# Optimization experiments

Hardware: AMD Instinct MI355X
Metric: run time of the kernel (lower is better)

The kernel has to match this reference:

```python
import jax, jax.numpy as jnp
import numpy as np
from jax import lax

EPS = 1e-5
NUM_HEADS = 8
HEAD_DIM = 64
NUM_DEVICES = 8
MAX_DEV = 3       # max_devices_per_token
TOP_K = 6         # num_experts_per_tok
EBF, DBF, CBF = 0.003, 0.05, 0.02  # aux loss factors


def rms_norm(x, eps=EPS):
    xf = x.astype(jnp.float32)
    var = jnp.mean(jnp.square(xf), axis=-1, keepdims=True)
    return (xf * lax.rsqrt(var + eps)).astype(x.dtype)


def rotate_half(x):
    x1, x2 = jnp.split(x, 2, axis=-1)
    return jnp.concatenate([-x2, x1], axis=-1)


def swiglu(x, wgu, wd):
    gate, up = jnp.split(x @ wgu, 2, axis=-1)
    return (jax.nn.silu(gate) * up) @ wd


def attention(x, w_qkv, w_o, cos, sin):
    B, S, H = x.shape
    qkv = (x @ w_qkv).reshape(B, S, 3 * NUM_HEADS, HEAD_DIM)
    q, k, v = (qkv[:, :, :NUM_HEADS], qkv[:, :, NUM_HEADS:2 * NUM_HEADS],
               qkv[:, :, 2 * NUM_HEADS:])
    c = cos[None, :, None, :]
    s = sin[None, :, None, :]
    q = q * c + rotate_half(q) * s
    k = k * c + rotate_half(k) * s
    scores = jnp.einsum('bqhd,bkhd->bhqk', q, k) / np.float32(np.sqrt(HEAD_DIM))
    p = jax.nn.softmax(scores, axis=-1)  # non-causal
    o = jnp.einsum('bhqk,bkhd->bqhd', p, v).reshape(B, S, H)
    return o @ w_o


def deepseek_moe(x, router_w, r_wgu, r_wd, s_wgu, s_wd):
    B, S, H = x.shape
    E = router_w.shape[1]
    epd = E // NUM_DEVICES
    e2d = jnp.arange(E) // epd  # expert -> device (contiguous blocks)

    logits = x @ router_w                         # [B,S,E]
    probs = jax.nn.softmax(logits, axis=-1)
    # device-limited routing (max_devices_per_token < num_devices)
    dev_scores = probs.reshape(B, S, NUM_DEVICES, epd).sum(-1)  # [B,S,D]
    _, sel_dev = lax.top_k(dev_scores, MAX_DEV)                 # [B,S,3]
    allowed = (sel_dev[..., :, None] == e2d[None, None, None, :]).any(-2)  # [B,S,E]
    masked = jnp.where(allowed, probs, -jnp.inf)
    w, idx = lax.top_k(masked, TOP_K)             # [B,S,K]
    w = jax.nn.softmax(w, axis=-1)

    T = B * S
    xf = x.reshape(T, H)
    idx_f = idx.reshape(T, TOP_K)
    # combine weights [T,E]: scatter-add top-k weights per token
    cw = jnp.zeros((T, E), x.dtype).at[jnp.arange(T)[:, None], idx_f].add(
        w.reshape(T, TOP_K))
    # accumulate weighted expert outputs, streaming one expert at a time
    def body(acc, we):
        wgu, wd, c = we
        return acc + c[:, None] * swiglu(xf, wgu, wd), None
    routed, _ = lax.scan(body, jnp.zeros_like(xf), (r_wgu, r_wd, cw.T))
    routed = routed.reshape(B, S, H)

    shared = swiglu(x, s_wgu[0], s_wd[0]) + swiglu(x, s_wgu[1], s_wd[1])
    out = x + shared + routed

    # auxiliary losses
    f_i = jnp.zeros(E, jnp.float32).at[idx.reshape(-1)].add(1.0) / (T * TOP_K)
    P_i = probs.astype(jnp.float32).mean((0, 1))
    expert_bal = (f_i * P_i).sum() * EBF
    dev_f = f_i.reshape(NUM_DEVICES, epd).mean(-1)
    dev_P = P_i.reshape(NUM_DEVICES, epd).sum(-1)
    device_bal = (dev_f * dev_P).sum() * DBF
    dev_sel = e2d[idx]  # [B,S,K]
    counts = jnp.zeros(NUM_DEVICES, jnp.float32).at[dev_sel.reshape(-1)].add(1.0)
    f_comm = counts / (T * MAX_DEV)
    comm_bal = (f_comm * dev_P).sum() * CBF
    return out, expert_bal, device_bal, comm_bal


def setup_inputs() -> dict:
    key = jax.random.key(0)
    ks = jax.random.split(key, 8)
    B, S, H, E = 4, 1024, 512, 64
    INTER = 1536  # _find_multiple(round(512*4*2/3), 256)
    sc = 1.0 / np.sqrt(H)
    sci = 1.0 / np.sqrt(INTER)
    # RoPE tables
    inv_freq = 1.0 / (10000.0 ** (np.arange(0, HEAD_DIM, 2) / HEAD_DIM))
    freqs = np.outer(np.arange(S), inv_freq)
    emb = np.concatenate([freqs, freqs], axis=-1)
    return {
        'hidden_states': jax.random.normal(ks[0], (B, S, H), jnp.float32),
        'cos': jnp.asarray(np.cos(emb), jnp.float32),
        'sin': jnp.asarray(np.sin(emb), jnp.float32),
        'w_qkv': jax.random.normal(ks[1], (H, 3 * H), jnp.float32) * sc,
        'w_o': jax.random.normal(ks[2], (H, H), jnp.float32) * sc,
        'router_w': jax.random.normal(ks[3], (H, E), jnp.float32) * sc,
        'r_wgu': jax.random.normal(ks[4], (E, H, 2 * INTER), jnp.float32) * sc,
        'r_wd': jax.random.normal(ks[5], (E, INTER, H), jnp.float32) * sci,
        's_wgu': jax.random.normal(ks[6], (2, H, 2 * INTER), jnp.float32) * sc,
        's_wd': jax.random.normal(ks[7], (2, INTER, H), jnp.float32) * sci,
    }


def reference(hidden_states, cos, sin, w_qkv, w_o, router_w, r_wgu, r_wd,
              s_wgu, s_wd):
    h = rms_norm(hidden_states + attention(hidden_states, w_qkv, w_o, cos, sin))
    moe_out, ebl, dbl, cbl = deepseek_moe(h, router_w, r_wgu, r_wd, s_wgu, s_wd)
    h = rms_norm(moe_out)
    return h, ebl, dbl, cbl, ebl + dbl + cbl
```

## Files before the change

kernel.cpp:

```cpp
#include <hip/hip_runtime.h>
#include <math.h>

#define TOK   4096
#define SEQL  1024
#define HID   512
#define NEXP  64
#define FFI   1536

typedef short bf16x8v __attribute__((ext_vector_type(8)));
typedef float f32x4   __attribute__((ext_vector_type(4)));

__device__ __forceinline__ unsigned short f2bf(float f){
  unsigned int u = __float_as_uint(f);
  u += 0x7fffu + ((u >> 16) & 1u);
  return (unsigned short)(u >> 16);
}
__device__ __forceinline__ float bf2f(unsigned short s){
  return __uint_as_float(((unsigned int)s) << 16);
}
__device__ __forceinline__ void split2(float v, unsigned short& h, unsigned short& l){
  h = f2bf(v);
  l = f2bf(v - bf2f(h));
}
__device__ __forceinline__ void gload16(const void* g, void* l){
// ... 42 lines not shown
    for (int j=0;j<8;j++) split2(tile[rq+j][c], th[j], tl[j]);
    long long o = (long long)(c0+c)*R + r0 + rq;
    *(uint4*)&ohi[o] = *(uint4*)th;
    *(uint4*)&olo[o] = *(uint4*)tl;
  }
}

template<bool PAIRED>
__global__ __launch_bounds__(256) void kconvT(const float* __restrict__ in,
    unsigned short* __restrict__ out, int R, int C){
  __shared__ float tile[64][65];
  long long zb = (long long)blockIdx.z * R * C;
  int c0 = blockIdx.x*64, r0 = blockIdx.y*64;
  int tid = threadIdx.x;
  #pragma unroll
  for (int it=0; it<4; it++){
    int idx = it*256+tid; int r = idx>>4; int cq = (idx&15)*4;
    float4 v = *(const float4*)&in[zb + (long long)(r0+r)*C + c0 + cq];
    tile[r][cq]=v.x; tile[r][cq+1]=v.y; tile[r][cq+2]=v.z; tile[r][cq+3]=v.w;
  }
  __syncthreads();
  #pragma unroll
  for (int it=0; it<2; it++){
    int idx = it*256+tid; int c = idx>>3; int rq=(idx&7)*8;
    unsigned short tb[8] __attribute__((aligned(16)));
    #pragma unroll
    for (int j=0;j<8;j++) tb[j] = f2bf(tile[rq+j][c]);
    int cc = c0 + c;
    int orow = PAIRED ? ((cc < (C>>1)) ? 2*cc : 2*(cc-(C>>1))+1) : cc;
    *(uint4*)&out[zb + (long long)orow*R + r0 + rq] = *(uint4*)tb;
  }
}

template<int WM,int WN,int FM,int FN,int SPLIT>
__global__ __launch_bounds__(256) void gemm_x3(
    const unsigned short* __restrict__ Ahi, const unsigned short* __restrict__ Alo,
    const unsigned short* __restrict__ Bhi, const unsigned short* __restrict__ Blo,
    float* __restrict__ C, unsigned short* __restrict__ OH, unsigned short* __restrict__ OL,
    int K, int lda, int ldb, int ldc, float alpha,
    long long a1, long long a2, int adiv,
    long long b1, long long b2, int bdiv,
    long long c1, long long c2, int cdiv)
{
  constexpr int BM = WM*FM*16, BN = WN*FN*16;
  constexpr int AIT = (2*BM*4)/256, BIT = (2*BN*4)/256;
  int z = blockIdx.z;
  long long aoff = (long long)(z/adiv)*a1 + (long long)(z%adiv)*a2;
  long long boff = (long long)(z/bdiv)*b1 + (long long)(z%bdiv)*b2;
  long long coff = (long long)(z/cdiv)*c1 + (long long)(z%cdiv)*c2;
  int m0 = blockIdx.x*BM, n0 = blockIdx.y*BN;
  __shared__ __align__(16) unsigned short As[2][BM*40];
  __shared__ __align__(16) unsigned short Bs[2][BN*40];
  int tid = threadIdx.x, lane = tid&63, wid = tid>>6;
  int wr = wid / WN, wc = wid % WN;
  int lrow = lane&15, kgo = (lane>>4)*8;
  f32x4 acc[FM][FN];
  #pragma unroll
  for (int mi=0;mi<FM;mi++)
    #pragma unroll
    for (int nj=0;nj<FN;nj++) acc[mi][nj] = (f32x4){0.f,0.f,0.f,0.f};

  for (int k0=0; k0<K; k0+=32){
    uint4 ta[AIT], tb[BIT];
    #pragma unroll
    for (int it=0; it<AIT; it++){
      int c = it*256+tid; int pl = c/(BM*4); int rem = c%(BM*4);
      int row = rem>>2, q = (rem&3)*8;
      const unsigned short* src = pl ? Alo : Ahi;
      ta[it] = *(const uint4*)&src[aoff + (long long)(m0+row)*lda + k0 + q];
    }
    #pragma unroll
// ... 17 lines not shown
      *(uint4*)&Bs[pl][row*40+q] = tb[it];
    }
    __syncthreads();
    bf16x8v ah[FM], al[FM], bh[FN], bl[FN];
    int ab = (wr*FM*16 + lrow)*40 + kgo;
    int bb = (wc*FN*16 + lrow)*40 + kgo;
    #pragma unroll
    for (int mi=0;mi<FM;mi++){
      ah[mi] = *(const bf16x8v*)&As[0][ab + mi*640];
      al[mi] = *(const bf16x8v*)&As[1][ab + mi*640];
    }
    #pragma unroll
    for (int nj=0;nj<FN;nj++){
      bh[nj] = *(const bf16x8v*)&Bs[0][bb + nj*640];
      bl[nj] = *(const bf16x8v*)&Bs[1][bb + nj*640];
    }
    #pragma unroll
    for (int mi=0;mi<FM;mi++)
      #pragma unroll
      for (int nj=0;nj<FN;nj++){
        acc[mi][nj] = __builtin_amdgcn_mfma_f32_16x16x32_bf16(ah[mi], bh[nj], acc[mi][nj], 0,0,0);
        acc[mi][nj] = __builtin_amdgcn_mfma_f32_16x16x32_bf16(ah[mi], bl[nj], acc[mi][nj], 0,0,0);
        acc[mi][nj] = __builtin_amdgcn_mfma_f32_16x16x32_bf16(al[mi], bh[nj], acc[mi][nj], 0,0,0);
      }
  }
  int crow = m0 + wr*FM*16 + ((lane>>4)<<2);
  int ccol = n0 + wc*FN*16 + (lane&15);
  #pragma unroll
  for (int mi=0;mi<FM;mi++)
    #pragma unroll
    for (int r=0;r<4;r++){
      long long row = crow + mi*16 + r;
      #pragma unroll
      for (int nj=0;nj<FN;nj++){
        float v = alpha*acc[mi][nj][r];
        if constexpr (SPLIT){
          unsigned short hh, ll;
          split2(v, hh, ll);
          OH[coff + row*ldc + ccol + nj*16] = hh;
          OL[coff + row*ldc + ccol + nj*16] = ll;
        } else {
          C[coff + row*ldc + ccol + nj*16] = v;
        }
      }
    }
}

__global__ __launch_bounds__(256) void krope(float* __restrict__ qkv,
    unsigned short* __restrict__ qhi, unsigned short* __restrict__ qlo,
    const float* __restrict__ cosb, const float* __restrict__ sinb){
  int gid = blockIdx.x*256 + threadIdx.x;
  int t = gid >> 8; int rem = gid & 255; int h = rem >> 5; int d = rem & 31;
  int s = t & (SEQL-1);
  long long base = (long long)t*1536 + h*64;
  float c1 = cosb[s*64+d], c2 = cosb[s*64+d+32];
  float s1 = sinb[s*64+d], s2 = sinb[s*64+d+32];
  float q1 = qkv[base+d], q2 = qkv[base+d+32];
  float rq1 = q1*c1 - q2*s1, rq2 = q2*c2 + q1*s2;
  qkv[base+d] = rq1; qkv[base+d+32] = rq2;
  split2(rq1, qhi[base+d],    qlo[base+d]);
  split2(rq2, qhi[base+d+32], qlo[base+d+32]);
  float k1 = qkv[base+512+d], k2 = qkv[base+512+d+32];
  float rk1 = k1*c1 - k2*s1, rk2 = k2*c2 + k1*s2;
  qkv[base+512+d] = rk1; qkv[base+512+d+32] = rk2;
  split2(rk1, qhi[base+512+d],    qlo[base+512+d]);
  split2(rk2, qhi[base+512+d+32], qlo[base+512+d+32]);
}

__global__ __launch_bounds__(256) void kvtrans(const float* __restrict__ qkv,
    unsigned short* __restrict__ vhi, unsigned short* __restrict__ vlo){
  __shared__ float tile[64][65];
  int s0 = blockIdx.x*64;
  int z = blockIdx.y;
  int b = z >> 3, h = z & 7;
  int tid = threadIdx.x;
  #pragma unroll
  for (int it=0; it<4; it++){
    int idx = it*256+tid; int r = idx>>4; int cq = (idx&15)*4;
    float4 v = *(const float4*)&qkv[((long long)(b*1024 + s0 + r))*1536 + 1024 + h*64 + cq];
    tile[r][cq]=v.x; tile[r][cq+1]=v.y; tile[r][cq+2]=v.z; tile[r][cq+3]=v.w;
  }
  __syncthreads();
  #pragma unroll
  for (int it=0; it<2; it++){
    int idx = it*256+tid; int d = idx>>3; int sq = (idx&7)*8;
    unsigned short th[8] __attribute__((aligned(16)));
    unsigned short tl[8] __attribute__((aligned(16)));
    #pragma unroll
    for (int j=0;j<8;j++) split2(tile[sq+j][d], th[j], tl[j]);
    long long o = ((long long)(z*64 + d))*1024 + s0 + sq;
    *(uint4*)&vhi[o] = *(uint4*)th;
    *(uint4*)&vlo[o] = *(uint4*)tl;
  }
}

__global__ __launch_bounds__(256) void ksoftmax(const float* __restrict__ sc,
    unsigned short* __restrict__ phi, unsigned short* __restrict__ plo){
  long long row = blockIdx.x;
  const float* p = sc + row*1024;
  int tid = threadIdx.x;
  float4 v = *(const float4*)&p[tid*4];
  float m = fmaxf(fmaxf(v.x,v.y), fmaxf(v.z,v.w));
  for (int o=32;o>0;o>>=1) m = fmaxf(m, __shfl_xor(m,o));
  __shared__ float redm[4], reds[4];
  int wid = tid>>6, lane = tid&63;
  if (lane==0) redm[wid]=m;
  __syncthreads();
  m = fmaxf(fmaxf(redm[0],redm[1]), fmaxf(redm[2],redm[3]));
  float e0=expf(v.x-m), e1=expf(v.y-m), e2=expf(v.z-m), e3=expf(v.w-m);
  float sum = e0+e1+e2+e3;
  for (int o=32;o>0;o>>=1) sum += __shfl_xor(sum,o);
  if (lane==0) reds[wid]=sum;
  __syncthreads();
  sum = reds[0]+reds[1]+reds[2]+reds[3];
  float inv = 1.0f/sum;
  unsigned short h0,h1,h2,h3,l0,l1,l2,l3;
  split2(e0*inv,h0,l0); split2(e1*inv,h1,l1); split2(e2*inv,h2,l2); split2(e3*inv,h3,l3);
  *(ushort4*)&phi[row*1024 + tid*4] = make_ushort4(h0,h1,h2,h3);
  *(ushort4*)&plo[row*1024 + tid*4] = make_ushort4(l0,l1,l2,l3);
}

__global__ __launch_bounds__(128) void krms1(const float* __restrict__ x, const float* __restrict__ attn,
    unsigned short* __restrict__ h1hi, unsigned short* __restrict__ h1lo,
    unsigned short* __restrict__ h1b, float* __restrict__ hbuf){
  long long row = blockIdx.x;
  int tid = threadIdx.x;
  float4 xv = *(const float4*)&x[row*512 + tid*4];
  float4 av = *(const float4*)&attn[row*512 + tid*4];
  float4 v; v.x=xv.x+av.x; v.y=xv.y+av.y; v.z=xv.z+av.z; v.w=xv.w+av.w;
  float ss = v.x*v.x + v.y*v.y + v.z*v.z + v.w*v.w;
  for (int o=32;o>0;o>>=1) ss += __shfl_xor(ss,o);
  __shared__ float red[2];
  int wid = tid>>6, lane = tid&63;
  if (lane==0) red[wid]=ss;
  __syncthreads();
  ss = red[0]+red[1];
  float r = 1.0f/sqrtf(ss*(1.0f/512.0f) + 1e-5f);
  float4 o; o.x=v.x*r; o.y=v.y*r; o.z=v.z*r; o.w=v.w*r;
  *(float4*)&hbuf[row*512 + tid*4] = o;
  unsigned short h0,h1,h2,h3,l0,l1,l2,l3;
  split2(o.x,h0,l0); split2(o.y,h1,l1); split2(o.z,h2,l2); split2(o.w,h3,l3);
  *(ushort4*)&h1hi[row*512 + tid*4] = make_ushort4(h0,h1,h2,h3);
  *(ushort4*)&h1lo[row*512 + tid*4] = make_ushort4(l0,l1,l2,l3);
  *(ushort4*)&h1b[row*512 + tid*4] = make_ushort4(f2bf(o.x),f2bf(o.y),f2bf(o.z),f2bf(o.w));
}

__device__ void route_decide(float p, int e, int t,
    int* __restrict__ idx, float* __restrict__ wts,
    int* __restrict__ flagcnt, int* __restrict__ flaglist){
  float d = p;
  d += __shfl_xor(d,1); d += __shfl_xor(d,2); d += __shfl_xor(d,4);
  int g = e >> 3;
  float gs[8];
  #pragma unroll
  for (int j=0;j<8;j++) gs[j] = __shfl(d, j*8);
  int rank = 0;
  #pragma unroll
  for (int j=0;j<8;j++) rank += (gs[j] > d) || (gs[j] == d && j < g);
  float q = (rank < 3) ? p : -INFINITY;
  float svals[7]; int sidx[7];
  #pragma unroll
  for (int kk=0; kk<7; kk++){
    float v = q; int vi = e;
    for (int o=32;o>0;o>>=1){
      float ov = __shfl_xor(v,o); int oi = __shfl_xor(vi,o);
      if (ov > v || (ov == v && oi < vi)){ v = ov; vi = oi; }
    }
    svals[kk] = v; sidx[kk] = vi;
    if (e == vi) q = -INFINITY;
  }
  float mx = svals[0], tot = 0.f, wv[6];
  #pragma unroll
  for (int kk=0;kk<6;kk++){ wv[kk] = expf(svals[kk]-mx); tot += wv[kk]; }
  if (e < 6){
    idx[t*6+e] = sidx[e];
    wts[t*6+e] = wv[e]/tot;
  }
  if (flagcnt != nullptr && e == 0){
    float a[8];
    #pragma unroll
    for (int j=0;j<8;j++) a[j] = gs[j];
    float t3=-1e30f, t4=-1e30f;
    for (int it2=0; it2<4; it2++){
      int bi=0; float bv=a[0];
      #pragma unroll
      for (int j=1;j<8;j++) if (a[j] > bv){ bv=a[j]; bi=j; }
      if (it2==2) t3=bv;
      if (it2==3) t4=bv;
      a[bi] = -1e30f;
    }
    float pgap = svals[5] - svals[6];
    float dgap = t3 - t4;
    if (pgap < 1e-4f || dgap < 5e-4f){
      int pos = atomicAdd(flagcnt, 1);
      if (pos < 1024) flaglist[pos] = t;
    }
  }
}

__global__ __launch_bounds__(256) void krouter(const float* __restrict__ logits,
    float* __restrict__ probs, int* __restrict__ idx, float* __restrict__ wts,
    int* __restrict__ flagcnt, int* __restrict__ flaglist){
  int t = blockIdx.x*4 + (threadIdx.x >> 6);
  int e = threadIdx.x & 63;
  float l = logits[t*64 + e];
  float m = l;
  for (int o=32;o>0;o>>=1) m = fmaxf(m, __shfl_xor(m,o));
  float p = expf(l-m);
  float s = p;
  for (int o=32;o>0;o>>=1) s += __shfl_xor(s,o);
  p /= s;
  probs[t*64+e] = p;
  route_decide(p, e, t, idx, wts, flagcnt, flaglist);
}

__global__ __launch_bounds__(256) void kfix_attn(const int* __restrict__ flagcnt,
    const int* __restrict__ flaglist, const float* __restrict__ qkv, float* __restrict__ fixo){
  int fc = *flagcnt; if (fc > 1024) fc = 1024;
  if ((int)blockIdx.x >= fc) return;
  int t = flaglist[blockIdx.x];
  int h = blockIdx.y;
  int b = t >> 10;
  int tid = threadIdx.x, lane = tid & 63, w = tid >> 6;
  __shared__ float sc[1024];
  __shared__ float qh[64];
  __shared__ float red[4];
  __shared__ float op[4][64];
  __shared__ float sinv;
  if (tid < 64) qh[tid] = qkv[(long long)t*1536 + h*64 + tid];
  __syncthreads();
  float q = qh[lane];
  const float* kb = qkv + (long long)b*1024*1536 + 512 + h*64 + lane;
  for (int s0 = w*256; s0 < w*256 + 256; s0 += 8){
    float p[8];
    #pragma unroll
    for (int j=0;j<8;j++) p[j] = q * kb[(long long)(s0+j)*1536];
    #pragma unroll
    for (int o=32;o>0;o>>=1){
      #pragma unroll
      for (int j=0;j<8;j++) p[j] += __shfl_xor(p[j],o);
    }
    if (lane == 0){
      #pragma unroll
      for (int j=0;j<8;j++) sc[s0+j] = p[j] * 0.125f;
    }
  }
// ... 1 lines not shown
  float m = -1e30f;
  for (int s = tid; s < 1024; s += 256) m = fmaxf(m, sc[s]);
  #pragma unroll
  for (int o=32;o>0;o>>=1) m = fmaxf(m, __shfl_xor(m,o));
  if (lane == 0) red[w] = m;
  __syncthreads();
  m = fmaxf(fmaxf(red[0],red[1]), fmaxf(red[2],red[3]));
  __syncthreads();
  float sum = 0.f;
  for (int s = tid; s < 1024; s += 256){ float e = expf(sc[s]-m); sc[s] = e; sum += e; }
  #pragma unroll
  for (int o=32;o>0;o>>=1) sum += __shfl_xor(sum,o);
  if (lane == 0) red[w] = sum;
  __syncthreads();
  if (tid == 0) sinv = 1.0f/(red[0]+red[1]+red[2]+red[3]);
  const float* vb = qkv + (long long)b*1024*1536 + 1024 + h*64 + lane;
  float a0 = 0.f, a1 = 0.f, a2 = 0.f, a3 = 0.f;
  for (int s = w*256; s < w*256 + 256; s += 4){
    a0 += sc[s]   * vb[(long long)(s)*1536];
    a1 += sc[s+1] * vb[(long long)(s+1)*1536];
    a2 += sc[s+2] * vb[(long long)(s+2)*1536];
    a3 += sc[s+3] * vb[(long long)(s+3)*1536];
  }
  op[w][lane] = (a0+a1)+(a2+a3);
  __syncthreads();
  if (tid < 64)
    fixo[(long long)blockIdx.x*512 + h*64 + tid] =
      (op[0][tid]+op[1][tid]+op[2][tid]+op[3][tid]) * sinv;
}

__global__ __launch_bounds__(256) void kfix_route(const int* __restrict__ flagcnt,
    const int* __restrict__ flaglist, const float* __restrict__ fixo,
    const float* __restrict__ x, const float* __restrict__ w_o, const float* __restrict__ router_w,
    int* __restrict__ idx, float* __restrict__ wts, float* __restrict__ probs){
  int fc = *flagcnt; if (fc > 1024) fc = 1024;
  if ((int)blockIdx.x >= fc) return;
  int t = flaglist[blockIdx.x];
  int tid = threadIdx.x;
  __shared__ float o512[512];
  __shared__ float h1s[512];
  __shared__ float red[4];
  o512[tid]     = fixo[(long long)blockIdx.x*512 + tid];
  o512[tid+256] = fixo[(long long)blockIdx.x*512 + tid + 256];
  __syncthreads();
  int j0 = tid, j1 = tid + 256;
  float a0 = 0.f, a1 = 0.f;
  #pragma unroll 4
  for (int i = 0; i < 512; i++){
    float oi = o512[i];
    a0 += oi * w_o[(long long)i*512 + j0];
    a1 += oi * w_o[(long long)i*512 + j1];
  }
  float hj0 = x[(long long)t*512 + j0] + a0;
  float hj1 = x[(long long)t*512 + j1] + a1;
  float ss = hj0*hj0 + hj1*hj1;
  #pragma unroll
  for (int o=32;o>0;o>>=1) ss += __shfl_xor(ss,o);
  if ((tid&63)==0) red[tid>>6]=ss;
  __syncthreads();
  ss = red[0]+red[1]+red[2]+red[3];
  float r = 1.0f/sqrtf(ss*(1.0f/512.0f) + 1e-5f);
  h1s[j0] = hj0*r; h1s[j1] = hj1*r;
  __syncthreads();
  if (tid < 64){
    int e = tid;
    float le = 0.f;
    #pragma unroll 4
    for (int i=0;i<512;i++) le += h1s[i]*router_w[(long long)i*64 + e];
    float m2 = le;
    #pragma unroll
    for (int o=32;o>0;o>>=1) m2 = fmaxf(m2, __shfl_xor(m2,o));
    float p = expf(le - m2), s2 = p;
    #pragma unroll
    for (int o=32;o>0;o>>=1) s2 += __shfl_xor(s2,o);
    p /= s2;
    probs[(long long)t*64 + e] = p;
    route_decide(p, e, t, idx, wts, nullptr, nullptr);
  }
}

__global__ void kcount(const int* __restrict__ idx, int* __restrict__ cnt){
  int g = blockIdx.x*256 + threadIdx.x;
  if (g < TOK*6) atomicAdd(&cnt[idx[g]], 1);
}

__global__ __launch_bounds__(256) void ksump(const float* __restrict__ probs, float* __restrict__ sumP){
  int e = blockIdx.x; int tid = threadIdx.x;
  float acc = 0.f;
  for (int t = tid; t < TOK; t += 256) acc += probs[t*64 + e];
  for (int o=32;o>0;o>>=1) acc += __shfl_xor(acc,o);
  __shared__ float red[4];
  int wid = tid>>6, lane = tid&63;
  if (lane==0) red[wid]=acc;
  __syncthreads();
  if (tid==0) sumP[e] = red[0]+red[1]+red[2]+red[3];
}

__global__ void kfinalize(const int* __restrict__ cnt, int* __restrict__ offs,
                          int2* __restrict__ tiles, int* __restrict__ ntl){
  int e = threadIdx.x;
  int c = cnt[e];
  int inc = c;
  #pragma unroll
  for (int o=1;o<64;o<<=1){ int v = __shfl_up(inc,o); if (e>=o) inc += v; }
  offs[e] = inc - c;
  if (e == 63) offs[64] = inc;
  int nte = (c + 127) >> 7;
  int tinc = nte;
  #pragma unroll
  for (int o=1;o<64;o<<=1){ int v = __shfl_up(tinc,o); if (e>=o) tinc += v; }
  int tbase = tinc - nte;
  for (int i=0;i<nte;i++) tiles[tbase+i] = make_int2(e, i*128);
  if (e == 63) *ntl = tinc;
}

__global__ __launch_bounds__(256) void kscatter(const int* __restrict__ idx, const float* __restrict__ wts,
    const int* __restrict__ offs, int* __restrict__ cursor,
    int* __restrict__ rowsl, float* __restrict__ wrowl, int* __restrict__ slot_of){
  int g = blockIdx.x*256 + threadIdx.x;
  if (g >= TOK*6) return;
  int t = g/6, kk = g%6;
  int e = idx[t*6+kk];
  int pos = atomicAdd(&cursor[e], 1);
  int slot = offs[e]+pos;
  rowsl[slot] = t;
  wrowl[slot] = wts[t*6+kk];
  slot_of[t*6+kk] = slot;
}

__global__ __launch_bounds__(256) void kgather(const unsigned short* __restrict__ h1b,
    const int* __restrict__ rowsl, unsigned short* __restrict__ xg){
  int r = blockIdx.x*4 + (threadIdx.x>>6);
  int lane = threadIdx.x&63;
  int tok = rowsl[r];
  *(uint4*)&xg[(long long)r*512 + lane*8] = *(const uint4*)&h1b[(long long)tok*512 + lane*8];
}

template<int MODE>
__global__ __launch_bounds__(256) void gemm_ffn(
    const unsigned short* __restrict__ Ab, const unsigned short* __restrict__ Bw,
    unsigned short* __restrict__ Cact, float* __restrict__ Cd,
    const int* __restrict__ offs, const int2* __restrict__ tiles, const int* __restrict__ ntl,
    int N, int K)
{
  int e=0, m0=0, roff=0, Me=1<<30, n0=0, zi=0;
  long long Aoff=0, Boff=0;
  int lda;
  if constexpr (MODE==0 || MODE==1){
    constexpr int NF = (MODE==0) ? 24 : 4;
    int nt = *ntl;
    int total = nt*NF;
    int l = xcd_swizzle(blockIdx.x, total);
    if (l < 0 || l >= total) return;
    int tile = l / NF; int y = l % NF;
    int2 tl = tiles[tile];
    e = tl.x; m0 = tl.y;
    roff = offs[e]; Me = offs[e+1]-roff;
    n0 = y*128;
    Boff = (long long)e*N*K;
    lda = K;
  } else {
    m0 = blockIdx.x*128;
    n0 = blockIdx.y*128;
    zi = blockIdx.z;
    Boff = (long long)zi*N*K;
    if constexpr (MODE==2) lda = 512;
    else { lda = K; Aoff = (long long)zi*4096LL*K; }
  }
  __shared__ __align__(16) unsigned short As[128*32];
  __shared__ __align__(16) unsigned short Bs[128*32];
  int tid = threadIdx.x, lane = tid&63, wid = tid>>6;
  int wr = wid>>1, wc = wid&1;
  int lrow = lane&15, kgo = (lane>>4)*8;
  f32x4 acc[4][4];
  #pragma unroll
  for (int mi=0;mi<4;mi++)
    #pragma unroll
    for (int nj=0;nj<4;nj++) acc[mi][nj] = (f32x4){0.f,0.f,0.f,0.f};

  int g0 = wid*2, g1 = wid*2 + 1;
  int colq = (lane&3)*8;
  int ar0 = g0*16 + (lane>>2), ar1 = g1*16 + (lane>>2);
  long long abase0, abase1;
  if constexpr (MODE==0 || MODE==1){
    int r0 = roff + m0 + ar0; if (r0 > 24575) r0 = 24575;
    int r1 = roff + m0 + ar1; if (r1 > 24575) r1 = 24575;
    abase0 = (long long)r0*lda; abase1 = (long long)r1*lda;
  } else if constexpr (MODE==2){
    abase0 = (long long)(m0+ar0)*lda; abase1 = (long long)(m0+ar1)*lda;
// ... 14 lines not shown
    int ab = (wr*64 + lrow)*32 + kgo;
    int bb = (wc*64 + lrow)*32 + kgo;
    #pragma unroll
    for (int mi=0;mi<4;mi++) af[mi]  = *(const bf16x8v*)&As[ab + mi*512];
    #pragma unroll
    for (int nj=0;nj<4;nj++) bfv[nj] = *(const bf16x8v*)&Bs[bb + nj*512];
    #pragma unroll
    for (int mi=0;mi<4;mi++)
      #pragma unroll
      for (int nj=0;nj<4;nj++)
        acc[mi][nj] = __builtin_amdgcn_mfma_f32_16x16x32_bf16(af[mi], bfv[nj], acc[mi][nj], 0,0,0);
  }

  int lq = lane>>4;
  int l15 = lane&15;
  if constexpr (MODE==0 || MODE==2){
    bool evenlane = (l15&1)==0;
    int pb = (n0>>1) + wc*32 + (l15>>1);
    #pragma unroll
    for (int mi=0;mi<4;mi++){
      #pragma unroll
      for (int r2=0;r2<4;r2++){
        int lr = wr*64 + mi*16 + lq*4 + r2;
        bool valid; long long grow;
        if constexpr (MODE==0){ valid = (m0+lr)<Me; grow = roff+m0+lr; }
        else { valid = true; grow = (long long)zi*4096 + m0 + lr; }
        #pragma unroll
        for (int nj=0;nj<4;nj++){
          float v = acc[mi][nj][r2];
          float o2 = __shfl_xor(v,1);
          if (evenlane && valid){
            float g = v, u = o2;
            float sg = g/(1.0f+expf(-g))*u;
            Cact[grow*1536 + pb + nj*8] = f2bf(sg);
          }
        }
      }
    }
  } else {
    #pragma unroll
    for (int mi=0;mi<4;mi++)
      #pragma unroll
      for (int r2=0;r2<4;r2++){
        int lr = wr*64 + mi*16 + lq*4 + r2;
        bool valid; long long grow;
        if constexpr (MODE==1){ valid = (m0+lr)<Me; grow = roff+m0+lr; }
        else { valid = true; grow = (long long)zi*4096 + m0 + lr; }
        if (valid){
          #pragma unroll
          for (int nj=0;nj<4;nj++)
            Cd[grow*512 + n0 + wc*64 + nj*16 + l15] = acc[mi][nj][r2];
        }
      }
  }
}

__global__ __launch_bounds__(128) void kreduce(const float* __restrict__ hbuf,
    const float* __restrict__ sdout, const float* __restrict__ dout,
    const int* __restrict__ slot_of, const float* __restrict__ wts,
    float* __restrict__ out){
  int t = blockIdx.x;
  int tid = threadIdx.x;
  int c4 = tid*4;
  float4 s = *(const float4*)&hbuf[(long long)t*512 + c4];
  float4 a = *(const float4*)&sdout[(long long)t*512 + c4];
  float4 b = *(const float4*)&sdout[(long long)(4096+t)*512 + c4];
  s.x += a.x + b.x; s.y += a.y + b.y; s.z += a.z + b.z; s.w += a.w + b.w;
  #pragma unroll
  for (int kk=0; kk<6; kk++){
    float w = wts[t*6+kk];
    int slot = slot_of[t*6+kk];
    float4 d = *(const float4*)&dout[(long long)slot*512 + c4];
    s.x += w*d.x; s.y += w*d.y; s.z += w*d.z; s.w += w*d.w;
  }
  float ss = s.x*s.x + s.y*s.y + s.z*s.z + s.w*s.w;
  for (int o=32;o>0;o>>=1) ss += __shfl_xor(ss,o);
  __shared__ float red[2];
  int wid = tid>>6, lane = tid&63;
  if (lane==0) red[wid]=ss;
  __syncthreads();
  ss = red[0]+red[1];
  float r = 1.0f/sqrtf(ss*(1.0f/512.0f) + 1e-5f);
  float4 o; o.x=s.x*r; o.y=s.y*r; o.z=s.z*r; o.w=s.w*r;
  *(float4*)&out[(long long)t*512 + c4] = o;
}

__global__ void kscalars(const int* __restrict__ cnt, const float* __restrict__ sumP, float* __restrict__ o){
  int e = threadIdx.x;
  float cf = (float)cnt[e];
  float f = cf / 24576.0f;
  float P = sumP[e] / 4096.0f;
  float fg = f, Pg = P, cg = cf;
  fg += __shfl_xor(fg,1); fg += __shfl_xor(fg,2); fg += __shfl_xor(fg,4);
  Pg += __shfl_xor(Pg,1); Pg += __shfl_xor(Pg,2); Pg += __shfl_xor(Pg,4);
  cg += __shfl_xor(cg,1); cg += __shfl_xor(cg,2); cg += __shfl_xor(cg,4);
  float t1 = f*P;
  float t2 = ((e&7)==0) ? (fg/8.0f)*Pg : 0.0f;
  float t3 = ((e&7)==0) ? (cg/12288.0f)*Pg : 0.0f;
  for (int s=32;s>0;s>>=1){
    t1 += __shfl_xor(t1,s); t2 += __shfl_xor(t2,s); t3 += __shfl_xor(t3,s);
  }
  if (e==0){
    float ebl = t1*0.003f, dbl = t2*0.05f, cbl = t3*0.02f;
    o[0]=ebl; o[1]=dbl; o[2]=cbl; o[3]=ebl+dbl+cbl;
  }
}
// ... 16 lines not shown
  char* base = (char*)d_ws;
  size_t off = 0;
  auto alloc = [&](size_t b)->char*{
    char* p = base + off; off = (off + b + 255) & ~(size_t)255; return p;
  };
  unsigned short* x_hi   = (unsigned short*)alloc(2097152ULL*2);
  unsigned short* x_lo   = (unsigned short*)alloc(2097152ULL*2);
  unsigned short* wqkvT_hi = (unsigned short*)alloc(786432ULL*2);
  unsigned short* wqkvT_lo = (unsigned short*)alloc(786432ULL*2);
  unsigned short* woT_hi = (unsigned short*)alloc(262144ULL*2);
  unsigned short* woT_lo = (unsigned short*)alloc(262144ULL*2);
  unsigned short* wrT_hi = (unsigned short*)alloc(32768ULL*2);
  unsigned short* wrT_lo = (unsigned short*)alloc(32768ULL*2);
  unsigned short* h1_hi  = (unsigned short*)alloc(2097152ULL*2);
  unsigned short* h1_lo  = (unsigned short*)alloc(2097152ULL*2);
  unsigned short* h1b    = (unsigned short*)alloc(2097152ULL*2);
  float* hbuf   = (float*)alloc(2097152ULL*4);
  float* fixo   = (float*)alloc(1024ULL*512*4);
  float* logits = (float*)alloc(262144ULL*4);
  float* probs  = (float*)alloc(262144ULL*4);
  int*   idx    = (int*)alloc(24576ULL*4);
  float* wts    = (float*)alloc(24576ULL*4);
  int*   slot_of= (int*)alloc(24576ULL*4);
  int*   cnt     = (int*)alloc(256);
  int*   cursor  = (int*)alloc(256);
  int*   flagcnt = (int*)alloc(256);
  int*   flaglist= (int*)alloc(1024*4);
  int*   offs   = (int*)alloc(65*4);
  int*   ntl    = (int*)alloc(256);
  float* sumP   = (float*)alloc(64*4);
  int2*  tiles  = (int2*)alloc(512*8);
  int*   rowsl  = (int*)alloc(24576ULL*4);
  float* wrowl  = (float*)alloc(24576ULL*4);

  size_t region = off;
  size_t oA = region, oF = region;
  auto allocV = [&](size_t b, size_t& o2)->char*{
    char* p = base + o2; o2 = (o2 + b + 255) & ~(size_t)255; return p;
  };
  float* qkv    = (float*)allocV(6291456ULL*4, oA);
  unsigned short* qkv_hi = (unsigned short*)allocV(6291456ULL*2, oA);
  unsigned short* qkv_lo = (unsigned short*)allocV(6291456ULL*2, oA);
  unsigned short* vT_hi  = (unsigned short*)allocV(2097152ULL*2, oA);
  unsigned short* vT_lo  = (unsigned short*)allocV(2097152ULL*2, oA);
  float* scores = (float*)allocV(33554432ULL*4, oA);
  unsigned short* p_hi = (unsigned short*)allocV(33554432ULL*2, oA);
  unsigned short* p_lo = (unsigned short*)allocV(33554432ULL*2, oA);
  unsigned short* attno_hi = (unsigned short*)allocV(2097152ULL*2, oA);
  unsigned short* attno_lo = (unsigned short*)allocV(2097152ULL*2, oA);
  float* attnw = (float*)allocV(2097152ULL*4, oA);
  unsigned short* wguT = (unsigned short*)allocV(100663296ULL*2, oF);
  unsigned short* sguT = (unsigned short*)allocV(3145728ULL*2, oF);
  unsigned short* xg   = (unsigned short*)allocV(12582912ULL*2, oF);
  unsigned short* hact = (unsigned short*)allocV(37748736ULL*2, oF);
  unsigned short* shact= (unsigned short*)allocV(12582912ULL*2, oF);
  float* dout  = (float*)allocV(12582912ULL*4, oF);
  float* sdout = (float*)allocV(4194304ULL*4, oF);
  unsigned short* wdT  = wguT;
  unsigned short* swdT = wguT + 50331648ULL;

  hipMemsetAsync(cnt, 0, 768, stream);

  ksplit<<<2048, 256, 0, stream>>>(x, x_hi, x_lo, 524288);
  kTsplit<<<dim3(24,8), 256, 0, stream>>>(w_qkv, wqkvT_hi, wqkvT_lo, 512, 1536);
  kTsplit<<<dim3(8,8),  256, 0, stream>>>(w_o, woT_hi, woT_lo, 512, 512);
  kTsplit<<<dim3(1,8),  256, 0, stream>>>(router_w, wrT_hi, wrT_lo, 512, 64);

  gemm_x3<2,2,4,4,0><<<dim3(32,12,1), 256, 0, stream>>>(x_hi, x_lo, wqkvT_hi, wqkvT_lo,
      qkv, nullptr, nullptr, 512, 512, 512, 1536, 1.0f, 0,0,1, 0,0,1, 0,0,1);
  krope<<<4096, 256, 0, stream>>>(qkv, qkv_hi, qkv_lo, cosb, sinb);
  kvtrans<<<dim3(16,32), 256, 0, stream>>>(qkv, vT_hi, vT_lo);

  gemm_x3<2,2,4,4,0><<<dim3(8,8,32), 256, 0, stream>>>(qkv_hi, qkv_lo, qkv_hi+512, qkv_lo+512,
      scores, nullptr, nullptr, 64, 1536, 1536, 1024, 0.125f,
      1572864LL,64,8, 1572864LL,64,8, 1048576LL,0,1);
  ksoftmax<<<32768, 256, 0, stream>>>(scores, p_hi, p_lo);
  gemm_x3<2,2,2,2,1><<<dim3(16,1,32), 256, 0, stream>>>(p_hi, p_lo, vT_hi, vT_lo,
      nullptr, attno_hi, attno_lo, 1024, 1024, 1024, 512, 1.0f,
      1048576LL,0,1, 65536LL,0,1, 524288LL,64,8);
  gemm_x3<2,2,4,4,0><<<dim3(32,4,1), 256, 0, stream>>>(attno_hi, attno_lo, woT_hi, woT_lo,
      attnw, nullptr, nullptr, 512, 512, 512, 512, 1.0f, 0,0,1, 0,0,1, 0,0,1);
  krms1<<<4096, 128, 0, stream>>>(x, attnw, h1_hi, h1_lo, h1b, hbuf);
  gemm_x3<2,2,2,2,0><<<dim3(64,1,1), 256, 0, stream>>>(h1_hi, h1_lo, wrT_hi, wrT_lo,
      logits, nullptr, nullptr, 512, 512, 512, 64, 1.0f, 0,0,1, 0,0,1, 0,0,1);
  krouter<<<1024, 256, 0, stream>>>(logits, probs, idx, wts, flagcnt, flaglist);
  kfix_attn<<<dim3(1024,8), 256, 0, stream>>>(flagcnt, flaglist, qkv, fixo);
  kfix_route<<<1024, 256, 0, stream>>>(flagcnt, flaglist, fixo, x, w_o, router_w, idx, wts, probs);
  kcount<<<96, 256, 0, stream>>>(idx, cnt);
  ksump<<<64, 256, 0, stream>>>(probs, sumP);
  kfinalize<<<1, 64, 0, stream>>>(cnt, offs, tiles, ntl);
  kscatter<<<96, 256, 0, stream>>>(idx, wts, offs, cursor, rowsl, wrowl, slot_of);

  kgather<<<6144, 256, 0, stream>>>(h1b, rowsl, xg);
  kconvT<true><<<dim3(48,8,64), 256, 0, stream>>>(r_wgu, wguT, 512, 3072);
  kconvT<true><<<dim3(48,8,2),  256, 0, stream>>>(s_wgu, sguT, 512, 3072);
  gemm_ffn<0><<<6144, 256, 0, stream>>>(xg, wguT, hact, nullptr, offs, tiles, ntl, 3072, 512);
  gemm_ffn<2><<<dim3(32,24,2), 256, 0, stream>>>(h1b, sguT, shact, nullptr, offs, tiles, ntl, 3072, 512);
  kconvT<false><<<dim3(8,24,64), 256, 0, stream>>>(r_wd, wdT, 1536, 512);
  kconvT<false><<<dim3(8,24,2),  256, 0, stream>>>(s_wd, swdT, 1536, 512);
  gemm_ffn<1><<<1024, 256, 0, stream>>>(hact, wdT, nullptr, dout, offs, tiles, ntl, 512, 1536);
  gemm_ffn<3><<<dim3(32,4,2), 256, 0, stream>>>(shact, swdT, nullptr, sdout, offs, tiles, ntl, 512, 1536);

  kreduce<<<4096, 128, 0, stream>>>(hbuf, sdout, dout, slot_of, wts, out);
  kscalars<<<1, 64, 0, stream>>>(cnt, sumP, out + 2097152);
}
```

Before: 1.379 ms.

## Fuse attention into flash kernel, fold expert counting into router, store FFN outputs bf16

Replaces the separate scores GEMM, softmax and PV GEMM with a single flash-attention kernel that keeps scores in registers and shared memory, using an online softmax with split-bf16 MFMAs. This removes the large fp32 score buffer and the two bf16 probability buffers. Expert counting moves into the router via atomics, with corrections in the fix-up kernel, so the separate count kernel is gone. The down-projection outputs are also stored as bf16 instead of fp32, which halves that traffic but lowers output precision. The buffer allocation changes from overlapped regions to separate allocations.

```diff
diff --git a/kernel.cpp b/kernel.cpp
--- a/kernel.cpp
+++ b/kernel.cpp
@@ -98,11 +98,11 @@
   }
 }
 
-template<int WM,int WN,int FM,int FN,int SPLIT>
+template<int WM,int WN,int FM,int FN>
 __global__ __launch_bounds__(256) void gemm_x3(
     const unsigned short* __restrict__ Ahi, const unsigned short* __restrict__ Alo,
     const unsigned short* __restrict__ Bhi, const unsigned short* __restrict__ Blo,
-    float* __restrict__ C, unsigned short* __restrict__ OH, unsigned short* __restrict__ OL,
+    float* __restrict__ C,
     int K, int lda, int ldb, int ldc, float alpha,
     long long a1, long long a2, int adiv,
     long long b1, long long b2, int bdiv,
@@ -186,17 +186,8 @@
     for (int r=0;r<4;r++){
       long long row = crow + mi*16 + r;
       #pragma unroll
-      for (int nj=0;nj<FN;nj++){
-        float v = alpha*acc[mi][nj][r];
-        if constexpr (SPLIT){
-          unsigned short hh, ll;
-          split2(v, hh, ll);
-          OH[coff + row*ldc + ccol + nj*16] = hh;
-          OL[coff + row*ldc + ccol + nj*16] = ll;
-        } else {
-          C[coff + row*ldc + ccol + nj*16] = v;
-        }
-      }
+      for (int nj=0;nj<FN;nj++)
+        C[coff + row*ldc + ccol + nj*16] = alpha*acc[mi][nj][r];
     }
 }
 
@@ -248,30 +239,116 @@
   }
 }
 
-__global__ __launch_bounds__(256) void ksoftmax(const float* __restrict__ sc,
-    unsigned short* __restrict__ phi, unsigned short* __restrict__ plo){
-  long long row = blockIdx.x;
-  const float* p = sc + row*1024;
-  int tid = threadIdx.x;
-  float4 v = *(const float4*)&p[tid*4];
-  float m = fmaxf(fmaxf(v.x,v.y), fmaxf(v.z,v.w));
-  for (int o=32;o>0;o>>=1) m = fmaxf(m, __shfl_xor(m,o));
-  __shared__ float redm[4], reds[4];
-  int wid = tid>>6, lane = tid&63;
-  if (lane==0) redm[wid]=m;
-  __syncthreads();
-  m = fmaxf(fmaxf(redm[0],redm[1]), fmaxf(redm[2],redm[3]));
-  float e0=expf(v.x-m), e1=expf(v.y-m), e2=expf(v.z-m), e3=expf(v.w-m);
-  float sum = e0+e1+e2+e3;
-  for (int o=32;o>0;o>>=1) sum += __shfl_xor(sum,o);
-  if (lane==0) reds[wid]=sum;
-  __syncthreads();
-  sum = reds[0]+reds[1]+reds[2]+reds[3];
-  float inv = 1.0f/sum;
-  unsigned short h0,h1,h2,h3,l0,l1,l2,l3;
-  split2(e0*inv,h0,l0); split2(e1*inv,h1,l1); split2(e2*inv,h2,l2); split2(e3*inv,h3,l3);
-  *(ushort4*)&phi[row*1024 + tid*4] = make_ushort4(h0,h1,h2,h3);
-  *(ushort4*)&plo[row*1024 + tid*4] = make_ushort4(l0,l1,l2,l3);
+__global__ __launch_bounds__(256) void kflash(
+    const unsigned short* __restrict__ qkv_hi, const unsigned short* __restrict__ qkv_lo,
+    const unsigned short* __restrict__ vT_hi,  const unsigned short* __restrict__ vT_lo,
+    unsigned short* __restrict__ attno_hi, unsigned short* __restrict__ attno_lo)
+{
+  int qt = blockIdx.x;
+  int z  = blockIdx.y;
+  int b = z >> 3, h = z & 7;
+  int tid = threadIdx.x, lane = tid & 63, w = tid >> 6;
+  int q0 = qt*64 + w*16;
+  int fr = lane & 15;
+  int fk = (lane >> 4) * 8;
+
+  long long qbase  = ((long long)(b*1024 + q0 + fr))*1536 + h*64;
+  long long kbhb   = ((long long)b*1024)*1536 + 512 + h*64;
+  long long vbase  = ((long long)z*64)*1024;
+
+  bf16x8v qa_h[2], qa_l[2];
+  qa_h[0] = *(const bf16x8v*)&qkv_hi[qbase + fk];
+  qa_h[1] = *(const bf16x8v*)&qkv_hi[qbase + 32 + fk];
+  qa_l[0] = *(const bf16x8v*)&qkv_lo[qbase + fk];
+  qa_l[1] = *(const bf16x8v*)&qkv_lo[qbase + 32 + fk];
+
+  __shared__ __align__(16) unsigned short Ph[4][16*64];
+  __shared__ __align__(16) unsigned short Pl[4][16*64];
+
+  float m_run[4], l_run[4];
+  #pragma unroll
+  for (int r=0;r<4;r++){ m_run[r] = -1e30f; l_run[r] = 0.f; }
+  f32x4 oacc[4];
+  #pragma unroll
+  for (int nj=0;nj<4;nj++) oacc[nj] = (f32x4){0.f,0.f,0.f,0.f};
+
+  for (int kt = 0; kt < 16; kt++){
+    int kv0 = kt*64;
+    f32x4 s[4];
+    #pragma unroll
+    for (int nj=0;nj<4;nj++) s[nj] = (f32x4){0.f,0.f,0.f,0.f};
+    #pragma unroll
+    for (int nj=0;nj<4;nj++){
+      long long kr = kbhb + (long long)(kv0 + nj*16 + fr)*1536;
+      #pragma unroll
+      for (int kd=0; kd<2; kd++){
+        bf16x8v kb_h = *(const bf16x8v*)&qkv_hi[kr + kd*32 + fk];
+        bf16x8v kb_l = *(const bf16x8v*)&qkv_lo[kr + kd*32 + fk];
+        s[nj] = __builtin_amdgcn_mfma_f32_16x16x32_bf16(qa_h[kd], kb_h, s[nj], 0,0,0);
+        s[nj] = __builtin_amdgcn_mfma_f32_16x16x32_bf16(qa_h[kd], kb_l, s[nj], 0,0,0);
+        s[nj] = __builtin_amdgcn_mfma_f32_16x16x32_bf16(qa_l[kd], kb_h, s[nj], 0,0,0);
+      }
+    }
+    #pragma unroll
+    for (int r=0;r<4;r++){
+      float mx = -1e30f;
+      #pragma unroll
+      for (int nj=0;nj<4;nj++){ s[nj][r] *= 0.125f; mx = fmaxf(mx, s[nj][r]); }
+      #pragma unroll
+      for (int o=1;o<16;o<<=1) mx = fmaxf(mx, __shfl_xor(mx, o));
+      float mnew = fmaxf(m_run[r], mx);
+      float sc = __expf(m_run[r] - mnew);
+      m_run[r] = mnew;
+      l_run[r] *= sc;
+      #pragma unroll
+      for (int nj=0;nj<4;nj++) oacc[nj][r] *= sc;
+    }
+    #pragma unroll
+    for (int nj=0;nj<4;nj++){
+      #pragma unroll
+      for (int r=0;r<4;r++){
+        float p = __expf(s[nj][r] - m_run[r]);
+        l_run[r] += p;
+        unsigned short ph, pl;
+        split2(p, ph, pl);
+        int row = (lane>>4)*4 + r;
+        int col = nj*16 + fr;
+        Ph[w][row*64+col] = ph;
+        Pl[w][row*64+col] = pl;
+      }
+    }
+    #pragma unroll
+    for (int ks=0; ks<2; ks++){
+      bf16x8v pa_h = *(const bf16x8v*)&Ph[w][fr*64 + ks*32 + fk];
+      bf16x8v pa_l = *(const bf16x8v*)&Pl[w][fr*64 + ks*32 + fk];
+      #pragma unroll
+      for (int nj=0;nj<4;nj++){
+        long long vr = vbase + (long long)(nj*16 + fr)*1024 + kv0 + ks*32 + fk;
+        bf16x8v vb_h = *(const bf16x8v*)&vT_hi[vr];
+        bf16x8v vb_l = *(const bf16x8v*)&vT_lo[vr];
+        oacc[nj] = __builtin_amdgcn_mfma_f32_16x16x32_bf16(pa_h, vb_h, oacc[nj], 0,0,0);
+        oacc[nj] = __builtin_amdgcn_mfma_f32_16x16x32_bf16(pa_h, vb_l, oacc[nj], 0,0,0);
+        oacc[nj] = __builtin_amdgcn_mfma_f32_16x16x32_bf16(pa_l, vb_h, oacc[nj], 0,0,0);
+      }
+    }
+  }
+  #pragma unroll
+  for (int r=0;r<4;r++){
+    float l = l_run[r];
+    #pragma unroll
+    for (int o=1;o<16;o<<=1) l += __shfl_xor(l, o);
+    float inv = 1.0f / l;
+    int row = (lane>>4)*4 + r;
+    long long tok = (long long)(b*1024 + qt*64 + w*16 + row);
+    #pragma unroll
+    for (int nj=0;nj<4;nj++){
+      float v = oacc[nj][r] * inv;
+      unsigned short hh, ll;
+      split2(v, hh, ll);
+      attno_hi[tok*512 + h*64 + nj*16 + fr] = hh;
+      attno_lo[tok*512 + h*64 + nj*16 + fr] = ll;
+    }
+  }
 }
 
 __global__ __launch_bounds__(128) void krms1(const float* __restrict__ x, const float* __restrict__ attn,
@@ -300,7 +377,7 @@
 }
 
 __device__ void route_decide(float p, int e, int t,
-    int* __restrict__ idx, float* __restrict__ wts,
+    int* __restrict__ idx, float* __restrict__ wts, int* __restrict__ cntp,
     int* __restrict__ flagcnt, int* __restrict__ flaglist){
   float d = p;
   d += __shfl_xor(d,1); d += __shfl_xor(d,2); d += __shfl_xor(d,4);
@@ -329,6 +406,7 @@
   if (e < 6){
     idx[t*6+e] = sidx[e];
     wts[t*6+e] = wv[e]/tot;
+    if (cntp) atomicAdd(&cntp[sidx[e]], 1);
   }
   if (flagcnt != nullptr && e == 0){
     float a[8];
@@ -354,7 +432,7 @@
 
 __global__ __launch_bounds__(256) void krouter(const float* __restrict__ logits,
     float* __restrict__ probs, int* __restrict__ idx, float* __restrict__ wts,
-    int* __restrict__ flagcnt, int* __restrict__ flaglist){
+    int* __restrict__ cnt, int* __restrict__ flagcnt, int* __restrict__ flaglist){
   int t = blockIdx.x*4 + (threadIdx.x >> 6);
   int e = threadIdx.x & 63;
   float l = logits[t*64 + e];
@@ -365,7 +443,7 @@
   for (int o=32;o>0;o>>=1) s += __shfl_xor(s,o);
   p /= s;
   probs[t*64+e] = p;
-  route_decide(p, e, t, idx, wts, flagcnt, flaglist);
+  route_decide(p, e, t, idx, wts, cnt, flagcnt, flaglist);
 }
 
 __global__ __launch_bounds__(256) void kfix_attn(const int* __restrict__ flagcnt,
@@ -433,7 +511,7 @@
 __global__ __launch_bounds__(256) void kfix_route(const int* __restrict__ flagcnt,
     const int* __restrict__ flaglist, const float* __restrict__ fixo,
     const float* __restrict__ x, const float* __restrict__ w_o, const float* __restrict__ router_w,
-    int* __restrict__ idx, float* __restrict__ wts, float* __restrict__ probs){
+    int* __restrict__ idx, float* __restrict__ wts, float* __restrict__ probs, int* __restrict__ cnt){
   int fc = *flagcnt; if (fc > 1024) fc = 1024;
   if ((int)blockIdx.x >= fc) return;
   int t = flaglist[blockIdx.x];
@@ -465,6 +543,7 @@
   __syncthreads();
   if (tid < 64){
     int e = tid;
+    if (e < 6) atomicSub(&cnt[idx[t*6+e]], 1);
     float le = 0.f;
     #pragma unroll 4
     for (int i=0;i<512;i++) le += h1s[i]*router_w[(long long)i*64 + e];
@@ -476,13 +555,8 @@
     for (int o=32;o>0;o>>=1) s2 += __shfl_xor(s2,o);
     p /= s2;
     probs[(long long)t*64 + e] = p;
-    route_decide(p, e, t, idx, wts, nullptr, nullptr);
-  }
-}
-
-__global__ void kcount(const int* __restrict__ idx, int* __restrict__ cnt){
-  int g = blockIdx.x*256 + threadIdx.x;
-  if (g < TOK*6) atomicAdd(&cnt[idx[g]], 1);
+    route_decide(p, e, t, idx, wts, cnt, nullptr, nullptr);
+  }
 }
 
 __global__ __launch_bounds__(256) void ksump(const float* __restrict__ probs, float* __restrict__ sumP){
@@ -540,11 +614,11 @@
 template<int MODE>
 __global__ __launch_bounds__(256) void gemm_ffn(
     const unsigned short* __restrict__ Ab, const unsigned short* __restrict__ Bw,
-    unsigned short* __restrict__ Cact, float* __restrict__ Cd,
+    unsigned short* __restrict__ Cout,
     const int* __restrict__ offs, const int2* __restrict__ tiles, const int* __restrict__ ntl,
     int N, int K)
 {
-  int e=0, m0=0, roff=0, Me=1<<30, n0=0, zi=0;
+  int m0=0, roff=0, Me=1<<30, n0=0, zi=0;
   long long Aoff=0, Boff=0;
   int lda;
   if constexpr (MODE==0 || MODE==1){
@@ -555,7 +629,7 @@
     if (l < 0 || l >= total) return;
     int tile = l / NF; int y = l % NF;
     int2 tl = tiles[tile];
-    e = tl.x; m0 = tl.y;
+    int e = tl.x; m0 = tl.y;
     roff = offs[e]; Me = offs[e+1]-roff;
     n0 = y*128;
     Boff = (long long)e*N*K;
@@ -636,7 +710,7 @@
           if (evenlane && valid){
             float g = v, u = o2;
             float sg = g/(1.0f+expf(-g))*u;
-            Cact[grow*1536 + pb + nj*8] = f2bf(sg);
+            Cout[grow*1536 + pb + nj*8] = f2bf(sg);
           }
         }
       }
@@ -653,29 +727,32 @@
         if (valid){
           #pragma unroll
           for (int nj=0;nj<4;nj++)
-            Cd[grow*512 + n0 + wc*64 + nj*16 + l15] = acc[mi][nj][r2];
+            Cout[grow*512 + n0 + wc*64 + nj*16 + l15] = f2bf(acc[mi][nj][r2]);
         }
       }
   }
 }
 
 __global__ __launch_bounds__(128) void kreduce(const float* __restrict__ hbuf,
-    const float* __restrict__ sdout, const float* __restrict__ dout,
+    const unsigned short* __restrict__ sdoutb, const unsigned short* __restrict__ doutb,
     const int* __restrict__ slot_of, const float* __restrict__ wts,
     float* __restrict__ out){
   int t = blockIdx.x;
   int tid = threadIdx.x;
   int c4 = tid*4;
   float4 s = *(const float4*)&hbuf[(long long)t*512 + c4];
-  float4 a = *(const float4*)&sdout[(long long)t*512 + c4];
-  float4 b = *(const float4*)&sdout[(long long)(4096+t)*512 + c4];
-  s.x += a.x + b.x; s.y += a.y + b.y; s.z += a.z + b.z; s.w += a.w + b.w;
+  ushort4 a = *(const ushort4*)&sdoutb[(long long)t*512 + c4];
+  ushort4 b2 = *(const ushort4*)&sdoutb[(long long)(4096+t)*512 + c4];
+  s.x += bf2f(a.x) + bf2f(b2.x);
+  s.y += bf2f(a.y) + bf2f(b2.y);
+  s.z += bf2f(a.z) + bf2f(b2.z);
+  s.w += bf2f(a.w) + bf2f(b2.w);
   #pragma unroll
   for (int kk=0; kk<6; kk++){
     float w = wts[t*6+kk];
     int slot = slot_of[t*6+kk];
-    float4 d = *(const float4*)&dout[(long long)slot*512 + c4];
-    s.x += w*d.x; s.y += w*d.y; s.z += w*d.z; s.w += w*d.w;
+    ushort4 d = *(const ushort4*)&doutb[(long long)slot*512 + c4];
+    s.x += w*bf2f(d.x); s.y += w*bf2f(d.y); s.z += w*bf2f(d.z); s.w += w*bf2f(d.w);
   }
   float ss = s.x*s.x + s.y*s.y + s.z*s.z + s.w*s.w;
   for (int o=32;o>0;o>>=1) ss += __shfl_xor(ss,o);
@@ -758,32 +835,23 @@
   int2*  tiles  = (int2*)alloc(512*8);
   int*   rowsl  = (int*)alloc(24576ULL*4);
   float* wrowl  = (float*)alloc(24576ULL*4);
-
-  size_t region = off;
-  size_t oA = region, oF = region;
-  auto allocV = [&](size_t b, size_t& o2)->char*{
-    char* p = base + o2; o2 = (o2 + b + 255) & ~(size_t)255; return p;
-  };
-  float* qkv    = (float*)allocV(6291456ULL*4, oA);
-  unsigned short* qkv_hi = (unsigned short*)allocV(6291456ULL*2, oA);
-  unsigned short* qkv_lo = (unsigned short*)allocV(6291456ULL*2, oA);
-  unsigned short* vT_hi  = (unsigned short*)allocV(2097152ULL*2, oA);
-  unsigned short* vT_lo  = (unsigned short*)allocV(2097152ULL*2, oA);
-  float* scores = (float*)allocV(33554432ULL*4, oA);
-  unsigned short* p_hi = (unsigned short*)allocV(33554432ULL*2, oA);
-  unsigned short* p_lo = (unsigned short*)allocV(33554432ULL*2, oA);
-  unsigned short* attno_hi = (unsigned short*)allocV(2097152ULL*2, oA);
-  unsigned short* attno_lo = (unsigned short*)allocV(2097152ULL*2, oA);
-  float* attnw = (float*)allocV(2097152ULL*4, oA);
-  unsigned short* wguT = (unsigned short*)allocV(100663296ULL*2, oF);
-  unsigned short* sguT = (unsigned short*)allocV(3145728ULL*2, oF);
-  unsigned short* xg   = (unsigned short*)allocV(12582912ULL*2, oF);
-  unsigned short* hact = (unsigned short*)allocV(37748736ULL*2, oF);
-  unsigned short* shact= (unsigned short*)allocV(12582912ULL*2, oF);
-  float* dout  = (float*)allocV(12582912ULL*4, oF);
-  float* sdout = (float*)allocV(4194304ULL*4, oF);
-  unsigned short* wdT  = wguT;
-  unsigned short* swdT = wguT + 50331648ULL;
+  float* qkv    = (float*)alloc(6291456ULL*4);
+  unsigned short* qkv_hi = (unsigned short*)alloc(6291456ULL*2);
+  unsigned short* qkv_lo = (unsigned short*)alloc(6291456ULL*2);
+  unsigned short* vT_hi  = (unsigned short*)alloc(2097152ULL*2);
+  unsigned short* vT_lo  = (unsigned short*)alloc(2097152ULL*2);
+  unsigned short* attno_hi = (unsigned short*)alloc(2097152ULL*2);
+  unsigned short* attno_lo = (unsigned short*)alloc(2097152ULL*2);
+  float* attnw = (float*)alloc(2097152ULL*4);
+  unsigned short* wguT = (unsigned short*)alloc(100663296ULL*2);
+  unsigned short* sguT = (unsigned short*)alloc(3145728ULL*2);
+  unsigned short* xg   = (unsigned short*)alloc(12582912ULL*2);
+  unsigned short* hact = (unsigned short*)alloc(37748736ULL*2);
+  unsigned short* shact= (unsigned short*)alloc(12582912ULL*2);
+  unsigned short* doutb  = (unsigned short*)alloc(12582912ULL*2);
+  unsigned short* sdoutb = (unsigned short*)alloc(4194304ULL*2);
+  unsigned short* wdT  = (unsigned short*)alloc(50331648ULL*2);
+  unsigned short* swdT = (unsigned short*)alloc(1572864ULL*2);
 
   hipMemsetAsync(cnt, 0, 768, stream);
 
@@ -792,27 +860,21 @@
   kTsplit<<<dim3(8,8),  256, 0, stream>>>(w_o, woT_hi, woT_lo, 512, 512);
   kTsplit<<<dim3(1,8),  256, 0, stream>>>(router_w, wrT_hi, wrT_lo, 512, 64);
 
-  gemm_x3<2,2,4,4,0><<<dim3(32,12,1), 256, 0, stream>>>(x_hi, x_lo, wqkvT_hi, wqkvT_lo,
-      qkv, nullptr, nullptr, 512, 512, 512, 1536, 1.0f, 0,0,1, 0,0,1, 0,0,1);
+  gemm_x3<2,2,4,4><<<dim3(32,12,1), 256, 0, stream>>>(x_hi, x_lo, wqkvT_hi, wqkvT_lo,
+      qkv, 512, 512, 512, 1536, 1.0f, 0,0,1, 0,0,1, 0,0,1);
   krope<<<4096, 256, 0, stream>>>(qkv, qkv_hi, qkv_lo, cosb, sinb);
   kvtrans<<<dim3(16,32), 256, 0, stream>>>(qkv, vT_hi, vT_lo);
 
-  gemm_x3<2,2,4,4,0><<<dim3(8,8,32), 256, 0, stream>>>(qkv_hi, qkv_lo, qkv_hi+512, qkv_lo+512,
-      scores, nullptr, nullptr, 64, 1536, 1536, 1024, 0.125f,
-      1572864LL,64,8, 1572864LL,64,8, 1048576LL,0,1);
-  ksoftmax<<<32768, 256, 0, stream>>>(scores, p_hi, p_lo);
-  gemm_x3<2,2,2,2,1><<<dim3(16,1,32), 256, 0, stream>>>(p_hi, p_lo, vT_hi, vT_lo,
-      nullptr, attno_hi, attno_lo, 1024, 1024, 1024, 512, 1.0f,
-      1048576LL,0,1, 65536LL,0,1, 524288LL,64,8);
-  gemm_x3<2,2,4,4,0><<<dim3(32,4,1), 256, 0, stream>>>(attno_hi, attno_lo, woT_hi, woT_lo,
-      attnw, nullptr, nullptr, 512, 512, 512, 512, 1.0f, 0,0,1, 0,0,1, 0,0,1);
+  kflash<<<dim3(16,32), 256, 0, stream>>>(qkv_hi, qkv_lo, vT_hi, vT_lo, attno_hi, attno_lo);
+
+  gemm_x3<2,2,4,4><<<dim3(32,4,1), 256, 0, stream>>>(attno_hi, attno_lo, woT_hi, woT_lo,
+      attnw, 512, 512, 512, 512, 1.0f, 0,0,1, 0,0,1, 0,0,1);
   krms1<<<4096, 128, 0, stream>>>(x, attnw, h1_hi, h1_lo, h1b, hbuf);
-  gemm_x3<2,2,2,2,0><<<dim3(64,1,1), 256, 0, stream>>>(h1_hi, h1_lo, wrT_hi, wrT_lo,
-      logits, nullptr, nullptr, 512, 512, 512, 64, 1.0f, 0,0,1, 0,0,1, 0,0,1);
-  krouter<<<1024, 256, 0, stream>>>(logits, probs, idx, wts, flagcnt, flaglist);
+  gemm_x3<2,2,2,2><<<dim3(64,1,1), 256, 0, stream>>>(h1_hi, h1_lo, wrT_hi, wrT_lo,
+      logits, 512, 512, 512, 64, 1.0f, 0,0,1, 0,0,1, 0,0,1);
+  krouter<<<1024, 256, 0, stream>>>(logits, probs, idx, wts, cnt, flagcnt, flaglist);
   kfix_attn<<<dim3(1024,8), 256, 0, stream>>>(flagcnt, flaglist, qkv, fixo);
-  kfix_route<<<1024, 256, 0, stream>>>(flagcnt, flaglist, fixo, x, w_o, router_w, idx, wts, probs);
-  kcount<<<96, 256, 0, stream>>>(idx, cnt);
+  kfix_route<<<1024, 256, 0, stream>>>(flagcnt, flaglist, fixo, x, w_o, router_w, idx, wts, probs, cnt);
   ksump<<<64, 256, 0, stream>>>(probs, sumP);
   kfinalize<<<1, 64, 0, stream>>>(cnt, offs, tiles, ntl);
   kscatter<<<96, 256, 0, stream>>>(idx, wts, offs, cursor, rowsl, wrowl, slot_of);
@@ -820,13 +882,13 @@
   kgather<<<6144, 256, 0, stream>>>(h1b, rowsl, xg);
   kconvT<true><<<dim3(48,8,64), 256, 0, stream>>>(r_wgu, wguT, 512, 3072);
   kconvT<true><<<dim3(48,8,2),  256, 0, stream>>>(s_wgu, sguT, 512, 3072);
-  gemm_ffn<0><<<6144, 256, 0, stream>>>(xg, wguT, hact, nullptr, offs, tiles, ntl, 3072, 512);
-  gemm_ffn<2><<<dim3(32,24,2), 256, 0, stream>>>(h1b, sguT, shact, nullptr, offs, tiles, ntl, 3072, 512);
+  gemm_ffn<0><<<6144, 256, 0, stream>>>(xg, wguT, hact, offs, tiles, ntl, 3072, 512);
+  gemm_ffn<2><<<dim3(32,24,2), 256, 0, stream>>>(h1b, sguT, shact, offs, tiles, ntl, 3072, 512);
   kconvT<false><<<dim3(8,24,64), 256, 0, stream>>>(r_wd, wdT, 1536, 512);
   kconvT<false><<<dim3(8,24,2),  256, 0, stream>>>(s_wd, swdT, 1536, 512);
-  gemm_ffn<1><<<1024, 256, 0, stream>>>(hact, wdT, nullptr, dout, offs, tiles, ntl, 512, 1536);
-  gemm_ffn<3><<<dim3(32,4,2), 256, 0, stream>>>(shact, swdT, nullptr, sdout, offs, tiles, ntl, 512, 1536);
-
-  kreduce<<<4096, 128, 0, stream>>>(hbuf, sdout, dout, slot_of, wts, out);
+  gemm_ffn<1><<<1024, 256, 0, stream>>>(hact, wdT, doutb, offs, tiles, ntl, 512, 1536);
+  gemm_ffn<3><<<dim3(32,4,2), 256, 0, stream>>>(shact, swdT, sdoutb, offs, tiles, ntl, 512, 1536);
+
+  kreduce<<<4096, 128, 0, stream>>>(hbuf, sdoutb, doutb, slot_of, wts, out);
   kscalars<<<1, 64, 0, stream>>>(cnt, sumP, out + 2097152);
 }
```

Measured after the change: 1.243 ms. 1.11x faster.
